# Performance work log

Measured on AMD Instinct MI355X. Metric: run time of the kernel, lower is better.

The kernel has to match this reference:

```python
import jax, jax.numpy as jnp
import numpy as np

S, D = 4096, 2048  # seq_len, embedding_space == qkv_dim


def setup_inputs() -> dict:
    key = jax.random.key(0)
    k1, k2, k3, k4, k5 = jax.random.split(key, 5)
    return {
        "input_embedding": jax.random.normal(k1, (S, D), dtype=jnp.float32),
        "query_embedding": jax.random.normal(k2, (S, D), dtype=jnp.float32),
        "Wq": jax.random.normal(k3, (D, D), dtype=jnp.float32) * 0.02,
        "Wk": jax.random.normal(k4, (D, D), dtype=jnp.float32) * 0.02,
        "Wv": jax.random.normal(k5, (D, D), dtype=jnp.float32) * 0.02,
        "include_mask": 0,  # False -> causal mask applied (module's inverted logic)
    }


def reference(input_embedding, query_embedding, Wq, Wk, Wv, include_mask):
    q = query_embedding @ Wq          # [S, D]
    k = input_embedding @ Wk          # [S, D]
    v = input_embedding @ Wv          # [S, D]
    scores = (q @ k.T) / 10.0         # [S, S]; module hardcodes /10, not sqrt(d)
    if not include_mask:
        # causal: -inf strictly above the diagonal (triu with offset 1)
        s = scores.shape[0]
        causal = jnp.tril(jnp.ones((s, s), dtype=bool))
        scores = jnp.where(causal, scores, -jnp.inf)
    probs = jax.nn.softmax(scores, axis=-1)
    return probs @ v                  # [S, D]
```

## Files before the change

### kernel.cpp

```cpp
#include <hip/hip_runtime.h>
#include <hip/hip_bf16.h>
#include <math.h>

typedef __bf16 bf16_t;
typedef __bf16 bf16x8 __attribute__((ext_vector_type(8)));
typedef float f32x4 __attribute__((ext_vector_type(4)));

enum { EP_BF16 = 0, EP_SCORES = 1, EP_F32 = 2, EP_F32A = 3, EP_I32A = 4 };

#define MEMFENCE asm volatile("" ::: "memory")
#define BARRIER() do { MEMFENCE; __builtin_amdgcn_s_barrier(); MEMFENCE; } while (0)

__device__ __forceinline__ void gload_lds16(const void* g, void* l) {
  __builtin_amdgcn_global_load_lds(
      (const __attribute__((address_space(1))) void*)g,
      (__attribute__((address_space(3))) void*)l, 16, 0, 0);
}

template <int N>
__device__ __forceinline__ void wait_vmcnt() {
  if constexpr (N == 0)       asm volatile("s_waitcnt vmcnt(0)" ::: "memory");
  else if constexpr (N == 6)  asm volatile("s_waitcnt vmcnt(6)" ::: "memory");
  else if constexpr (N == 8)  asm volatile("s_waitcnt vmcnt(8)" ::: "memory");
  else if constexpr (N == 12) asm volatile("s_waitcnt vmcnt(12)" ::: "memory");
  else static_assert(N == 0, "unsupported vmcnt");
}

__device__ __forceinline__ int xcd_swz(int bid, int nwg) {
  const int q = nwg >> 3;
  return (bid & 7) * q + (bid >> 3);
}


template <int TM, bool STG, int WAITN>
__device__ __forceinline__ void do_tile(char* smem, int slot, int sslot, size_t stoff,
                                        const char* const* gbase, const int* lbase,
                                        const int* aoff, const int* boff,
                                        f32x4 (&acc)[TM][4]) {
  bf16x8 bfr[4], af[4];
  if constexpr (TM == 8) {
#pragma unroll
    for (int n = 0; n < 4; ++n) bfr[n] = *(const bf16x8*)(smem + slot + boff[n]);
#pragma unroll
    for (int m = 0; m < 4; ++m) af[m] = *(const bf16x8*)(smem + slot + aoff[m]);
    if constexpr (STG) {
      gload_lds16(gbase[0] + stoff, smem + sslot + lbase[0]);
      gload_lds16(gbase[1] + stoff, smem + sslot + lbase[1]);
    }
    BARRIER();
    asm volatile("s_waitcnt lgkmcnt(0)" ::: "memory");
    __builtin_amdgcn_sched_barrier(0);
    __builtin_amdgcn_s_setprio(1);
#pragma unroll
    for (int m = 0; m < 4; ++m)
#pragma unroll
      for (int n = 0; n < 4; ++n)
        acc[m][n] = __builtin_amdgcn_mfma_f32_16x16x32_bf16(af[m], bfr[n], acc[m][n], 0, 0, 0);
    __builtin_amdgcn_s_setprio(0);
    BARRIER();
#pragma unroll
    for (int m = 0; m < 4; ++m) af[m] = *(const bf16x8*)(smem + slot + aoff[4 + m]);
    if constexpr (STG) {
      gload_lds16(gbase[2] + stoff, smem + sslot + lbase[2]);
      gload_lds16(gbase[3] + stoff, smem + sslot + lbase[3]);
      wait_vmcnt<WAITN>();
    }
    BARRIER();
    asm volatile("s_waitcnt lgkmcnt(0)" ::: "memory");
    __builtin_amdgcn_sched_barrier(0);
    __builtin_amdgcn_s_setprio(1);
#pragma unroll
    for (int m = 0; m < 4; ++m)
#pragma unroll
      for (int n = 0; n < 4; ++n)
        acc[4 + m][n] = __builtin_amdgcn_mfma_f32_16x16x32_bf16(af[m], bfr[n], acc[4 + m][n], 0, 0, 0);
    __builtin_amdgcn_s_setprio(0);
    BARRIER();
  } else {
#pragma unroll
    for (int n = 0; n < 4; ++n) bfr[n] = *(const bf16x8*)(smem + slot + boff[n]);
#pragma unroll
    for (int m = 0; m < 4; ++m) af[m] = *(const bf16x8*)(smem + slot + aoff[m]);
    if constexpr (STG) {
      gload_lds16(gbase[0] + stoff, smem + sslot + lbase[0]);
      gload_lds16(gbase[1] + stoff, smem + sslot + lbase[1]);
      gload_lds16(gbase[2] + stoff, smem + sslot + lbase[2]);
      wait_vmcnt<WAITN>();
    }
    BARRIER();
    asm volatile("s_waitcnt lgkmcnt(0)" ::: "memory");
    __builtin_amdgcn_sched_barrier(0);
    __builtin_amdgcn_s_setprio(1);
#pragma unroll
    for (int m = 0; m < 4; ++m)
#pragma unroll
      for (int n = 0; n < 4; ++n)
        acc[m][n] = __builtin_amdgcn_mfma_f32_16x16x32_bf16(af[m], bfr[n], acc[m][n], 0, 0, 0);
    __builtin_amdgcn_s_setprio(0);
    BARRIER();
  }
}

template <int TM, int EPI, int NSLOT>
__device__ __forceinline__ void gemm_core(
    const bf16_t* __restrict__ A, const bf16_t* __restrict__ B,
    void* __restrict__ Cout, int Nout, int kstride, int klen,
    int row0, int col0, bool causal, float scale, char* smem)
{
  constexpr int BM = TM * 32;
  constexpr int LPT_A = BM / 128;
  constexpr int LPT = LPT_A + 2;
  constexpr int ABYTES = BM * 64;
  constexpr int SLOT = (BM + 256) * 64;
  constexpr int DEPTH = NSLOT - 1;
  constexpr int WAITN = (DEPTH - 1) * LPT;

  const int tid = threadIdx.x;
  const int w = tid >> 6, lane = tid & 63;
  const int wr = w >> 2, wc = w & 3;

  const int nt = klen >> 5;

  const char* gbase[LPT];
  int lbase[LPT];
  {
    const int sd = (tid & 3) ^ ((tid >> 3) & 3);
    const int rrow = tid >> 2;
#pragma unroll
    for (int r = 0; r < LPT; ++r) {
      const bool isA = (r < LPT_A);
      const int rr = isA ? r : (r - LPT_A);
      const int grow = (isA ? row0 : col0) + rr * 128 + rrow;
      const bf16_t* op = isA ? A : B;
      gbase[r] = (const char*)(op + (size_t)grow * kstride) + sd * 16;
      lbase[r] = (isA ? 0 : ABYTES) + rr * 8192 + w * 1024;
    }
  }

  const int fl = lane & 15;
  const int arow_off = fl * 64 + (((lane >> 4) ^ ((fl >> 1) & 3)) * 16);
  int aoff[TM], boff[4];
#pragma unroll
  for (int m = 0; m < TM; ++m) aoff[m] = (wr * (TM * 16) + m * 16) * 64 + arow_off;
#pragma unroll
  for (int n = 0; n < 4; ++n) boff[n] = ABYTES + (wc * 64 + n * 16) * 64 + arow_off;

  f32x4 acc[TM][4] = {};

  const int npro = nt < DEPTH ? nt : DEPTH;
  for (int t = 0; t < npro; ++t)
#pragma unroll
    for (int r = 0; r < LPT; ++r)
      gload_lds16(gbase[r] + (size_t)t * 64, smem + (t % NSLOT) * SLOT + lbase[r]);

  const int nmain = nt - DEPTH;
  if (nmain > 0) {
    wait_vmcnt<WAITN>();
    BARRIER();
    for (int t = 0; t < nmain; ++t)
      do_tile<TM, true, WAITN>(smem, (t % NSLOT) * SLOT, ((t + DEPTH) % NSLOT) * SLOT,
                               (size_t)(t + DEPTH) * 64, gbase, lbase, aoff, boff, acc);
  }

  wait_vmcnt<0>();
  BARRIER();
  for (int t = nmain > 0 ? nmain : 0; t < nt; ++t)
    do_tile<TM, false, 0>(smem, (t % NSLOT) * SLOT, 0, 0, gbase, lbase, aoff, boff, acc);

  const int cr = (lane >> 4) * 4;
  const int cc = lane & 15;
#pragma unroll
  for (int m = 0; m < TM; ++m) {
#pragma unroll
    for (int n = 0; n < 4; ++n) {
#pragma unroll
      for (int i = 0; i < 4; ++i) {
        const int r = row0 + wr * (TM * 16) + m * 16 + cr + i;
        const int c = col0 + wc * 64 + n * 16 + cc;
        float v = acc[m][n][i];
        if (EPI == EP_BF16) {
          ((bf16_t*)Cout)[(size_t)r * Nout + c] = (bf16_t)v;
        } else if (EPI == EP_SCORES) {
          v *= scale;
          if (causal && c > r) v = -INFINITY;
          ((float*)Cout)[(size_t)r * Nout + c] = v;
        } else if (EPI == EP_F32) {
          ((float*)Cout)[(size_t)r * Nout + c] = v;
        } else if (EPI == EP_F32A) {
          atomicAdd((float*)Cout + (size_t)r * Nout + c, v);
        } else {
          atomicAdd((int*)Cout + (size_t)r * Nout + c,
                    __float2int_rn(v * 16777216.0f));
        }
      }
    }
  }
}

__launch_bounds__(512, 2)
__global__ void qk_k(const bf16_t* __restrict__ qe16, const bf16_t* __restrict__ ie16,
                     const bf16_t* __restrict__ WqT, const bf16_t* __restrict__ WkT,
                     bf16_t* __restrict__ q16, bf16_t* __restrict__ k16) {
  extern __shared__ __align__(16) char smem[];
  int wg = xcd_swz(blockIdx.x, gridDim.x);
  const bf16_t *A, *B; bf16_t* C;
  if (wg < 128) { A = qe16; B = WqT; C = q16; }
  else          { A = ie16; B = WkT; C = k16; wg -= 128; }
  const int row0 = (wg >> 3) * 256, col0 = (wg & 7) * 256;
  gemm_core<8, EP_BF16, 4>(A, B, C, 2048, 2048, 2048, row0, col0, false, 1.f, smem);
}

__launch_bounds__(512, 2)
__global__ void vs_k(const bf16_t* __restrict__ WvT, const bf16_t* __restrict__ ie16,
                     const bf16_t* __restrict__ q16, const bf16_t* __restrict__ k16,
                     bf16_t* __restrict__ vT16, float* __restrict__ scores,
                     const int* __restrict__ maskflag) {
  extern __shared__ __align__(16) char smem[];
  const bool causal = maskflag[0] == 0;
  const int nsc = causal ? 136 : 256;
  const int bid = blockIdx.x;
  if (bid < nsc) {
    const int sid = xcd_swz(bid, nsc);
    int r, c;
    if (causal) {
      r = (int)((sqrtf(8.f * (float)sid + 1.f) - 1.f) * 0.5f);
      while ((r + 1) * (r + 2) / 2 <= sid) ++r;
      while (r * (r + 1) / 2 > sid) --r;
      c = sid - r * (r + 1) / 2;
    } else {
      r = sid >> 4; c = sid & 15;
    }
    gemm_core<8, EP_SCORES, 4>(q16, k16, scores, 4096, 2048, 2048,
                               r * 256, c * 256, causal, 0.1f, smem);
  } else {
    const int j = bid - nsc;
    if (j >= 120) return;
    gemm_core<8, EP_BF16, 4>(WvT, ie16, vT16, 4096, 2048, 2048,
                             (j >> 4) * 256, (j & 15) * 256, false, 1.f, smem);
  }
}

__launch_bounds__(512, 2)
__global__ void smv3_k(const bf16_t* __restrict__ WvT, const bf16_t* __restrict__ ie16,
                       bf16_t* __restrict__ vT16, int* __restrict__ vT32i,
                       const float* __restrict__ scores, bf16_t* __restrict__ probs,
                       const int* __restrict__ maskflag) {
  extern __shared__ __align__(16) char smem[];
  const bool causal = maskflag[0] == 0;
  const int nv = causal ? 32 : 128;
  const int bid = blockIdx.x;
  if (bid < nv) {
    if (causal) {
      const int ov = bid & 7;
      const int piece = bid >> 3;
      const bf16_t* A = WvT + (size_t)1792 * 2048 + piece * 512;
      const bf16_t* B = ie16 + (size_t)(2048 + ov * 256) * 2048 + piece * 512;
      gemm_core<8, EP_I32A, 4>(A, B, vT32i + ov * 65536, 256, 2048, 512,
                               0, 0, false, 1.f, smem);
    } else {
      const int j = bid;
      gemm_core<8, EP_BF16, 4>(WvT, ie16, vT16, 4096, 2048, 2048,
                               (j >> 4) * 256, (j & 15) * 256, false, 1.f, smem);
    }
    return;
  }
  const int p = bid - nv;
  if (p >= 2048) return;
  const int tid = threadIdx.x;
  const int h = tid >> 8;
  const int t = tid & 255;
  const int row = 2 * p + h;
  const int L = causal ? (row + 1) : 4096;
  const float* srow = scores + (size_t)row * 4096;
  float v[16];
  float m = -INFINITY;
#pragma unroll
  for (int j = 0; j < 16; ++j) {
    const int idx = t + j * 256;
    v[j] = (idx < L) ? srow[idx] : -INFINITY;
    m = fmaxf(m, v[j]);
  }
#pragma unroll
  for (int off = 32; off >= 1; off >>= 1) m = fmaxf(m, __shfl_xor(m, off));
  __shared__ float redm[8];
  __shared__ float reds[8];
  if ((tid & 63) == 0) redm[tid >> 6] = m;
  __syncthreads();
  m = fmaxf(fmaxf(redm[4 * h + 0], redm[4 * h + 1]),
            fmaxf(redm[4 * h + 2], redm[4 * h + 3]));
  float s = 0.f;
#pragma unroll
  for (int j = 0; j < 16; ++j) {
    v[j] = __expf(v[j] - m);
    s += v[j];
  }
#pragma unroll
  for (int off = 32; off >= 1; off >>= 1) s += __shfl_xor(s, off);
  if ((tid & 63) == 0) reds[tid >> 6] = s;
  __syncthreads();
  s = reds[4 * h + 0] + reds[4 * h + 1] + reds[4 * h + 2] + reds[4 * h + 3];
  const float inv = 1.f / s;
  bf16_t* prow = probs + (size_t)row * 4096;
#pragma unroll
  for (int j = 0; j < 16; ++j) prow[t + j * 256] = (bf16_t)(v[j] * inv);
}

__global__ void cvt8_k(const int* __restrict__ vT32i, bf16_t* __restrict__ vT16,
                       const int* __restrict__ maskflag) {
  if (maskflag[0] != 0) return;
  const long i = ((long)blockIdx.x * blockDim.x + threadIdx.x) * 8;
  if (i >= 8L * 65536) return;
  const int tile = (int)(i >> 16);
  const int within = (int)(i & 65535);
  const int r = within >> 8, c = within & 255;
  const int4 a = *(const int4*)(vT32i + i);
  const int4 b = *(const int4*)(vT32i + i + 4);
  bf16x8 o;
  o[0] = (__bf16)((float)a.x * (1.0f / 16777216.0f));
  o[1] = (__bf16)((float)a.y * (1.0f / 16777216.0f));
  o[2] = (__bf16)((float)a.z * (1.0f / 16777216.0f));
  o[3] = (__bf16)((float)a.w * (1.0f / 16777216.0f));
  o[4] = (__bf16)((float)b.x * (1.0f / 16777216.0f));
  o[5] = (__bf16)((float)b.y * (1.0f / 16777216.0f));
  o[6] = (__bf16)((float)b.z * (1.0f / 16777216.0f));
  o[7] = (__bf16)((float)b.w * (1.0f / 16777216.0f));
  *(bf16x8*)(vT16 + (size_t)(1792 + r) * 4096 + (8 + tile) * 256 + c) = o;
}

__launch_bounds__(512, 2)
__global__ void pv_k(const bf16_t* __restrict__ probs, const bf16_t* __restrict__ vT16,
                     float* __restrict__ out, const int* __restrict__ maskflag) {
  extern __shared__ __align__(16) char smem[];
  const bool causal = maskflag[0] == 0;
  const int bid = blockIdx.x;
  if (causal) {
    if (bid >= 256) return;
    const int sid  = xcd_swz(bid, 256);
    const int half = sid & 1;
    const int pair = (sid >> 1) & 15;
    const int col  = sid >> 5;
    const int blo = pair, bhi = 31 - pair;
    const int Klo = 128 * (blo + 1);
    const int cut = 2112 - Klo;
    if (half == 0) {
      gemm_core<4, EP_F32, 6>(probs, vT16, out, 2048, 4096, Klo,
                              blo * 128, col * 256, false, 1.f, smem);
      __syncthreads();
      gemm_core<4, EP_F32A, 6>(probs, vT16, out, 2048, 4096, cut,
                               bhi * 128, col * 256, false, 1.f, smem);
    } else {
      gemm_core<4, EP_F32A, 6>(probs + cut, vT16 + cut, out, 2048, 4096, 2112,
                               bhi * 128, col * 256, false, 1.f, smem);
    }
  } else {
    if (bid >= 512) return;
    const int sid = xcd_swz(bid, 512);
    const int t = sid >> 1;
    const int band = t & 31, col = t >> 5;
    const int k0 = (sid & 1) ? 2048 : 0;
    gemm_core<4, EP_F32A, 6>(probs + k0, vT16 + k0, out, 2048, 4096, 2048,
                             band * 128, col * 256, false, 1.f, smem);
  }
}


__global__ void cvt_k(const float* __restrict__ qe, const float* __restrict__ ie,
                      bf16_t* __restrict__ qe16, bf16_t* __restrict__ ie16,
                      float* __restrict__ zout, float* __restrict__ zv, long n) {
  const int y = blockIdx.y;
  long i = ((long)blockIdx.x * blockDim.x + threadIdx.x) * 8;
  const long stride = (long)gridDim.x * blockDim.x * 8;
  if (y >= 2) {
    float* z = (y == 2) ? zout : zv;
    const long nz = (y == 2) ? n : 8L * 65536;
    const float4 zero4 = make_float4(0.f, 0.f, 0.f, 0.f);
    for (; i < nz; i += stride) {
      *(float4*)(z + i) = zero4;
      *(float4*)(z + i + 4) = zero4;
    }
    return;
  }
  const float* x = y ? ie : qe;
  bf16_t* o = y ? ie16 : qe16;
  for (; i < n; i += stride) {
    const float4 a = *(const float4*)(x + i);
    const float4 b = *(const float4*)(x + i + 4);
    bf16x8 u;
    u[0] = (__bf16)a.x; u[1] = (__bf16)a.y; u[2] = (__bf16)a.z; u[3] = (__bf16)a.w;
    u[4] = (__bf16)b.x; u[5] = (__bf16)b.y; u[6] = (__bf16)b.z; u[7] = (__bf16)b.w;
    *(bf16x8*)(o + i) = u;
  }
}

__global__ void trans_k(const float* __restrict__ Wq, const float* __restrict__ Wk,
                        const float* __restrict__ Wv,
                        bf16_t* __restrict__ WqT, bf16_t* __restrict__ WkT,
                        bf16_t* __restrict__ WvT, int Dm) {
  const float* W = blockIdx.z == 0 ? Wq : (blockIdx.z == 1 ? Wk : Wv);
  bf16_t* WT = blockIdx.z == 0 ? WqT : (blockIdx.z == 1 ? WkT : WvT);
  __shared__ float tile[32][33];
  const int bx = blockIdx.x, by = blockIdx.y;
  const int tx = threadIdx.x & 31, ty = threadIdx.x >> 5;
#pragma unroll
  for (int r = ty; r < 32; r += 8)
    tile[r][tx] = W[(size_t)(by * 32 + r) * Dm + bx * 32 + tx];
  __syncthreads();
#pragma unroll
  for (int r = ty; r < 32; r += 8)
    WT[(size_t)(bx * 32 + r) * Dm + by * 32 + tx] = (bf16_t)tile[tx][r];
}

extern "C" void kernel_launch(void* const* d_in, const int* in_sizes, int n_in,
                              void* d_out, int out_size, void* d_ws, size_t ws_size,
                              hipStream_t stream) {
  const float* ie = (const float*)d_in[0];
  const float* qe = (const float*)d_in[1];
  const float* Wq = (const float*)d_in[2];
  const float* Wk = (const float*)d_in[3];
  const float* Wv = (const float*)d_in[4];
  const int* mask = (const int*)d_in[5];
  float* out = (float*)d_out;

  const int S = 4096, D = 2048;
  char* ws = (char*)d_ws;
  const size_t MB = 1u << 20;
  bf16_t* q16  = (bf16_t*)(ws + 0 * MB);
  bf16_t* k16  = (bf16_t*)(ws + 16 * MB);
  bf16_t* vT16 = (bf16_t*)(ws + 32 * MB);
  bf16_t* ie16 = (bf16_t*)(ws + 48 * MB);
  bf16_t* WvT  = (bf16_t*)(ws + 64 * MB);
  bf16_t* qe16 = (bf16_t*)(ws + 72 * MB);
  bf16_t* WqT  = (bf16_t*)(ws + 88 * MB);
  bf16_t* WkT  = (bf16_t*)(ws + 96 * MB);
  float*  scores = (float*)(ws + 72 * MB);
  bf16_t* probs  = (bf16_t*)(ws + 0 * MB);
  float*  vT32   = (float*)(ws + 136 * MB);

  hipFuncSetAttribute(reinterpret_cast<const void*>(&qk_k),
                      hipFuncAttributeMaxDynamicSharedMemorySize, 131072);
  hipFuncSetAttribute(reinterpret_cast<const void*>(&vs_k),
                      hipFuncAttributeMaxDynamicSharedMemorySize, 131072);
  hipFuncSetAttribute(reinterpret_cast<const void*>(&smv3_k),
                      hipFuncAttributeMaxDynamicSharedMemorySize, 131072);
  hipFuncSetAttribute(reinterpret_cast<const void*>(&pv_k),
                      hipFuncAttributeMaxDynamicSharedMemorySize, 147456);

  cvt_k<<<dim3(1024, 4), 256, 0, stream>>>(qe, ie, qe16, ie16, out, vT32, (long)S * D);
  trans_k<<<dim3(D / 32, D / 32, 3), 256, 0, stream>>>(Wq, Wk, Wv, WqT, WkT, WvT, D);

  qk_k<<<256, 512, 131072, stream>>>(qe16, ie16, WqT, WkT, q16, k16);

  vs_k<<<256, 512, 131072, stream>>>(WvT, ie16, q16, k16, vT16, scores, mask);

  smv3_k<<<2176, 512, 131072, stream>>>(WvT, ie16, vT16, (int*)vT32, scores, probs, mask);

  cvt8_k<<<256, 256, 0, stream>>>((const int*)vT32, vT16, mask);

  pv_k<<<512, 512, 147456, stream>>>(probs, vT16, out, mask);
}
```

Baseline: 268.5 us.

## Replace GEMM core with 8-phase pipelined 256x256 bf16 MFMA loop

Adds a new GEMM core that splits each pair of 64-wide K tiles into eight phases. Each phase interleaves one quarter of the next tiles' global-to-LDS loads with its LDS fragment reads and MFMA work, using XOR-swizzled LDS addressing, raised wave priority during MFMAs, and vmcnt(4) waits. The QK projection, scores and V projection kernels switch to this core. The aim is to hide load latency and cut LDS bank conflicts, at the cost of many more barriers per tile and a dependence on K being a multiple of 128.

Result: slower. 274.9 us (+2.4%).

```diff
diff --git a/kernel.cpp b/kernel.cpp
--- a/kernel.cpp
+++ b/kernel.cpp
@@ -20,6 +20,7 @@
 template <int N>
 __device__ __forceinline__ void wait_vmcnt() {
   if constexpr (N == 0)       asm volatile("s_waitcnt vmcnt(0)" ::: "memory");
+  else if constexpr (N == 4)  asm volatile("s_waitcnt vmcnt(4)" ::: "memory");
   else if constexpr (N == 6)  asm volatile("s_waitcnt vmcnt(6)" ::: "memory");
   else if constexpr (N == 8)  asm volatile("s_waitcnt vmcnt(8)" ::: "memory");
   else if constexpr (N == 12) asm volatile("s_waitcnt vmcnt(12)" ::: "memory");
@@ -29,6 +30,129 @@
 __device__ __forceinline__ int xcd_swz(int bid, int nwg) {
   const int q = nwg >> 3;
   return (bid & 7) * q + (bid >> 3);
+}
+
+template <int EPI>
+__device__ __forceinline__ void g8_core(
+    const bf16_t* __restrict__ A, const bf16_t* __restrict__ B,
+    void* __restrict__ Cout, int Nout, int kstride, int klen,
+    int row0, int col0, bool causal, float scale, char* smem)
+{
+  const int tid = threadIdx.x;
+  const int w = tid >> 6, lane = tid & 63;
+  const int wr = w >> 2, wc = w & 3;
+  const size_t ks2 = (size_t)kstride * 2;
+
+  const int ls0 = ((tid & 7) ^ ((tid >> 3) & 7)) * 16;
+  const char* gA = (const char*)A + (size_t)(row0 + (tid >> 3)) * ks2 + ls0;
+  const char* gB = (const char*)B + (size_t)(col0 + (tid >> 3)) * ks2 + ls0;
+  const int ldsw = w * 1024;
+
+  const int abase = (wr * 128 + (lane & 15)) * 128;
+  const int bbase = 32768 + (wc * 64 + (lane & 15)) * 128;
+  const int ps0 = ((lane >> 4) ^ (lane & 7)) * 16;
+  const int ps1 = (((lane >> 4) + 4) ^ (lane & 7)) * 16;
+
+  f32x4 acc[8][4] = {};
+  bf16x8 bfr[4][2];
+
+  const int nt = klen >> 6;
+  const int niter = nt >> 1;
+
+  auto stg = [&](int tile, int half, bool isA) {
+    const int slot = (tile & 1) * 65536;
+    const char* gp = (isA ? gA : gB) + (size_t)(half * 128) * ks2 + (size_t)tile * 128;
+    char* lp = smem + slot + (isA ? 0 : 32768) + half * 16384 + ldsw;
+    gload_lds16(gp, lp);
+    gload_lds16(gp + 64 * ks2, lp + 8192);
+  };
+
+  stg(0, 0, false); stg(0, 1, false);
+  stg(0, 0, true);  stg(0, 1, true);
+  stg(1, 0, false); stg(1, 1, false);
+  wait_vmcnt<4>();
+  BARRIER();
+
+  for (int I = 0; I < niter; ++I) {
+    const int t = 2 * I;
+    const bool last = (I == niter - 1);
+#pragma unroll
+    for (int ph = 0; ph < 8; ++ph) {
+      const int tc = t + (ph >> 2);
+      const int slot = (tc & 1) * 65536;
+      const int q = ph & 3;
+      if (ph == 0 && I > 0) { wait_vmcnt<4>(); BARRIER(); }
+      if (ph == 4) {
+        if (!last) wait_vmcnt<4>(); else wait_vmcnt<0>();
+        BARRIER();
+      }
+      if (q == 0) {
+#pragma unroll
+        for (int nf = 0; nf < 4; ++nf) {
+          bfr[nf][0] = *(const bf16x8*)(smem + slot + bbase + nf * 2048 + ps0);
+          bfr[nf][1] = *(const bf16x8*)(smem + slot + bbase + nf * 2048 + ps1);
+        }
+      }
+      bf16x8 af[2][2];
+#pragma unroll
+      for (int m2 = 0; m2 < 2; ++m2) {
+        af[m2][0] = *(const bf16x8*)(smem + slot + abase + (2 * q + m2) * 2048 + ps0);
+        af[m2][1] = *(const bf16x8*)(smem + slot + abase + (2 * q + m2) * 2048 + ps1);
+      }
+      if (!last) {
+        switch (ph) {
+          case 0: stg(t + 1, 0, true);  break;
+          case 1: stg(t + 1, 1, true);  break;
+          case 2: stg(t + 2, 0, false); break;
+          case 3: stg(t + 2, 1, false); break;
+          case 4: stg(t + 2, 0, true);  break;
+          case 5: stg(t + 2, 1, true);  break;
+          case 6: stg(t + 3, 0, false); break;
+          case 7: stg(t + 3, 1, false); break;
+        }
+      } else {
+        if (ph == 0) stg(t + 1, 0, true);
+        else if (ph == 1) stg(t + 1, 1, true);
+      }
+      BARRIER();
+      asm volatile("s_waitcnt lgkmcnt(0)" ::: "memory");
+      __builtin_amdgcn_sched_barrier(0);
+      __builtin_amdgcn_s_setprio(1);
+#pragma unroll
+      for (int m2 = 0; m2 < 2; ++m2)
+#pragma unroll
+        for (int nf = 0; nf < 4; ++nf) {
+          acc[2 * q + m2][nf] = __builtin_amdgcn_mfma_f32_16x16x32_bf16(
+              af[m2][0], bfr[nf][0], acc[2 * q + m2][nf], 0, 0, 0);
+          acc[2 * q + m2][nf] = __builtin_amdgcn_mfma_f32_16x16x32_bf16(
+              af[m2][1], bfr[nf][1], acc[2 * q + m2][nf], 0, 0, 0);
+        }
+      __builtin_amdgcn_s_setprio(0);
+      BARRIER();
+    }
+  }
+
+  const int cr = (lane >> 4) * 4;
+  const int cc = lane & 15;
+#pragma unroll
+  for (int mf = 0; mf < 8; ++mf) {
+#pragma unroll
+    for (int nf = 0; nf < 4; ++nf) {
+#pragma unroll
+      for (int i = 0; i < 4; ++i) {
+        const int r = row0 + wr * 128 + mf * 16 + cr + i;
+        const int c = col0 + wc * 64 + nf * 16 + cc;
+        float v = acc[mf][nf][i];
+        if (EPI == EP_BF16) {
+          ((bf16_t*)Cout)[(size_t)r * Nout + c] = (bf16_t)v;
+        } else if (EPI == EP_SCORES) {
+          v *= scale;
+          if (causal && c > r) v = -INFINITY;
+          ((float*)Cout)[(size_t)r * Nout + c] = v;
+        }
+      }
+    }
+  }
 }
 
 
@@ -207,7 +331,7 @@
   if (wg < 128) { A = qe16; B = WqT; C = q16; }
   else          { A = ie16; B = WkT; C = k16; wg -= 128; }
   const int row0 = (wg >> 3) * 256, col0 = (wg & 7) * 256;
-  gemm_core<8, EP_BF16, 4>(A, B, C, 2048, 2048, 2048, row0, col0, false, 1.f, smem);
+  g8_core<EP_BF16>(A, B, C, 2048, 2048, 2048, row0, col0, false, 1.f, smem);
 }
 
 __launch_bounds__(512, 2)
@@ -230,13 +354,13 @@
     } else {
       r = sid >> 4; c = sid & 15;
     }
-    gemm_core<8, EP_SCORES, 4>(q16, k16, scores, 4096, 2048, 2048,
-                               r * 256, c * 256, causal, 0.1f, smem);
+    g8_core<EP_SCORES>(q16, k16, scores, 4096, 2048, 2048,
+                       r * 256, c * 256, causal, 0.1f, smem);
   } else {
     const int j = bid - nsc;
     if (j >= 120) return;
-    gemm_core<8, EP_BF16, 4>(WvT, ie16, vT16, 4096, 2048, 2048,
-                             (j >> 4) * 256, (j & 15) * 256, false, 1.f, smem);
+    g8_core<EP_BF16>(WvT, ie16, vT16, 4096, 2048, 2048,
+                     (j >> 4) * 256, (j & 15) * 256, false, 1.f, smem);
   }
 }
 
```
